# Kernel tuning notes

Hardware: AMD Instinct MI355X
Metric: run time of the kernel (lower is better)

The kernel has to match this reference:

```python
import jax, jax.numpy as jnp
import numpy as np

EMBED = 1024
HEADS = 16
HEAD_DIM = EMBED // HEADS


def setup_inputs() -> dict:
    key = jax.random.key(0)
    ks = jax.random.split(key, 8)
    N, S = 4, 2048
    inp = {
        "values": jax.random.normal(ks[0], (N, S, EMBED), jnp.float32),
        "keys": jax.random.normal(ks[1], (N, S, EMBED), jnp.float32),
        "queries": jax.random.normal(ks[2], (N, S, EMBED), jnp.float32),
        "mask": jnp.ones((N, S), jnp.int32),  # unused by the original forward
        # learned params (torch Linear: y = x @ W.T + b)
        "Wv": jax.random.normal(ks[3], (HEAD_DIM, HEAD_DIM), jnp.float32) / np.sqrt(HEAD_DIM),
        "Wk": jax.random.normal(ks[4], (HEAD_DIM, HEAD_DIM), jnp.float32) / np.sqrt(HEAD_DIM),
        "Wq": jax.random.normal(ks[5], (HEAD_DIM, HEAD_DIM), jnp.float32) / np.sqrt(HEAD_DIM),
        "Wo": jax.random.normal(ks[6], (EMBED, EMBED), jnp.float32) / np.sqrt(EMBED),
        "bo": jax.random.normal(ks[7], (EMBED,), jnp.float32) * 0.01,
    }
    return inp


def reference(values, keys, queries, mask, Wv, Wk, Wq, Wo, bo):
    N, S, _ = queries.shape
    # reshape to (N, len, heads, head_dim)
    v = values.reshape(N, S, HEADS, HEAD_DIM)
    k = keys.reshape(N, S, HEADS, HEAD_DIM)
    q = queries.reshape(N, S, HEADS, HEAD_DIM)
    # per-head linear projections (weights shared across heads), y = x @ W.T
    v = jnp.einsum('nlhd,ed->nlhe', v, Wv)
    k = jnp.einsum('nlhd,ed->nlhe', k, Wk)
    q = jnp.einsum('nlhd,ed->nlhe', q, Wq)
    # attention scores scaled by sqrt(embed_size), faithful to original
    scores = jnp.einsum('nqhd,nkhd->nhqk', q, k) / jnp.sqrt(jnp.float32(EMBED))
    attn = jax.nn.softmax(scores, axis=3)
    out = jnp.einsum('nhql,nlhd->nqhd', attn, v).reshape(N, S, EMBED)
    return out @ Wo.T + bo
```

## Files before the change

kernel.cpp:

```cpp
#include <hip/hip_runtime.h>


using f32x4  = __attribute__((ext_vector_type(4))) float;
using f32x16 = __attribute__((ext_vector_type(16))) float;
using bf16x8 = __attribute__((ext_vector_type(8))) __bf16;
using u32x4  = __attribute__((ext_vector_type(4))) unsigned int;
using u16x8  = __attribute__((ext_vector_type(8))) unsigned short;
typedef unsigned short u16;
typedef unsigned int   u32;
typedef unsigned long long u64;

#define SEQ 2048
#define EMB 1024
#define NHEADS 16
#define HDIM 64
#define NBATCH 4
#define NH 64

__device__ __forceinline__ u16 f2bf(float f) {
  u32 u = __builtin_bit_cast(u32, f);
  return (u16)((u + 0x7fffu + ((u >> 16) & 1u)) >> 16);
}

__device__ __forceinline__ u32 cvtpk_bf16(float a, float b) {
  u32 d;
  asm("v_cvt_pk_bf16_f32 %0, %1, %2" : "=v"(d) : "v"(a), "v"(b));
  return d;
}

__device__ __forceinline__ f32x4 mfma16(bf16x8 a, bf16x8 b, f32x4 c) {
  return __builtin_amdgcn_mfma_f32_16x16x32_bf16(a, b, c, 0, 0, 0);
}

__device__ __forceinline__ f32x16 mfma32(bf16x8 a, bf16x8 b, f32x16 c) {
  return __builtin_amdgcn_mfma_f32_32x32x16_bf16(a, b, c, 0, 0, 0);
}

__device__ __forceinline__ bf16x8 cvt8(f32x4 a, f32x4 b) {
  u32x4 r;
  r[0] = cvtpk_bf16(a[0], a[1]);
  r[1] = cvtpk_bf16(a[2], a[3]);
  r[2] = cvtpk_bf16(b[0], b[1]);
  r[3] = cvtpk_bf16(b[2], b[3]);
  return __builtin_bit_cast(bf16x8, r);
}

__device__ __forceinline__ float fexp2(float x) {
#if __has_builtin(__builtin_amdgcn_exp2f)
  return __builtin_amdgcn_exp2f(x);
#else
  return __expf(x * 0.6931471805599453f);
#endif
}

__device__ __forceinline__ void swap_words(u32 a, u32 b, int hi, u32& wlo, u32& whi) {
#if __has_builtin(__builtin_amdgcn_permlane32_swap)
  (void)hi;
  auto rr = __builtin_amdgcn_permlane32_swap((int)a, (int)b, false, false);
  wlo = (u32)rr[0];
  whi = (u32)rr[1];
#else
  u32 pa = (u32)__shfl_xor((int)a, 32);
  u32 pb = (u32)__shfl_xor((int)b, 32);
  wlo = hi ? pb : a;
  whi = hi ? b : pa;
#endif
}

__global__ __launch_bounds__(256) void proj_kernel(
    const float* __restrict__ Xq, const float* __restrict__ Xk, const float* __restrict__ Xv,
    const float* __restrict__ Wq, const float* __restrict__ Wk, const float* __restrict__ Wv,
    u16* __restrict__ Qp, u16* __restrict__ Kp, u16* __restrict__ Vp)
{
  int which = blockIdx.y;
  const float* X = which == 0 ? Xq : (which == 1 ? Xk : Xv);
  const float* W = which == 0 ? Wq : (which == 1 ? Wk : Wv);
  u16* Out = which == 0 ? Qp : (which == 1 ? Kp : Vp);
  float wscale = which == 0 ? 0.045084220027780106f : 1.0f;

  int t = threadIdx.x;
  int w = t >> 6, l = t & 63, l15 = l & 15, grp = l >> 4;
  int g0 = blockIdx.x * 64;

  bf16x8 wf[4][2];
#pragma unroll
  for (int nt = 0; nt < 4; nt++) {
    int c = nt * 16 + l15;
#pragma unroll
    for (int dc = 0; dc < 2; dc++) {
      const float* p = W + c * 64 + dc * 32 + grp * 8;
      f32x4 a = *(const f32x4*)p;
      f32x4 b = *(const f32x4*)(p + 4);
      a *= wscale; b *= wscale;
      wf[nt][dc] = cvt8(a, b);
    }
  }
  int grow = g0 + w * 16 + l15;
  const float* xr = X + (long)grow * 64;
  bf16x8 af[2];
#pragma unroll
  for (int dc = 0; dc < 2; dc++) {
    f32x4 a = *(const f32x4*)(xr + dc * 32 + grp * 8);
    f32x4 b = *(const f32x4*)(xr + dc * 32 + grp * 8 + 4);
    af[dc] = cvt8(a, b);
  }
  f32x4 acc[4] = {};
#pragma unroll
  for (int dc = 0; dc < 2; dc++)
#pragma unroll
    for (int nt = 0; nt < 4; nt++)
      acc[nt] = mfma16(af[dc], wf[nt][dc], acc[nt]);

#pragma unroll
  for (int r = 0; r < 4; r++) {
    int g = g0 + w * 16 + grp * 4 + r;
    int n = g >> 15;
    int s = (g >> 4) & 2047;
    int h = g & 15;
    u16* orow = Out + (((long)(n * NHEADS + h) * SEQ + s) << 6);
#pragma unroll
    for (int nt = 0; nt < 4; nt++)
      orow[nt * 16 + l15] = f2bf(acc[nt][r]);
  }
}

__global__ __launch_bounds__(256) void transpose_v(
    const u16* __restrict__ Vp, u16* __restrict__ Vt)
{
  int st = blockIdx.x;
  int nh = blockIdx.y;
  __shared__ u16 Vs[64 * 65];
  int t = threadIdx.x;
  const u16* src = Vp + ((long)nh * SEQ + st * 64) * 64;
#pragma unroll
  for (int p = 0; p < 2; p++) {
    int row = p * 32 + (t >> 3);
    int c0 = (t & 7) * 8;
    u32x4 u = *(const u32x4*)(src + row * 64 + c0);
    u16x8 v = __builtin_bit_cast(u16x8, u);
#pragma unroll
    for (int j = 0; j < 8; j++) Vs[(c0 + j) * 65 + row] = v[j];
  }
  __syncthreads();
  int e = t >> 2, k0 = (t & 3) * 16;
  u16x8 lo, hi;
#pragma unroll
  for (int j = 0; j < 8; j++) { lo[j] = Vs[e * 65 + k0 + j]; hi[j] = Vs[e * 65 + k0 + 8 + j]; }
  u16* dst = Vt + ((long)nh * 64 + e) * SEQ + st * 64 + k0;
  *(u32x4*)dst = __builtin_bit_cast(u32x4, lo);
  *(u32x4*)(dst + 8) = __builtin_bit_cast(u32x4, hi);
}

__global__ __launch_bounds__(256) void conv_wo(
    const float* __restrict__ Wo, u16* __restrict__ Wob)
{
  int i = (blockIdx.x * 256 + threadIdx.x) * 4;
  f32x4 v = *(const f32x4*)(Wo + i);
  u32 w0 = cvtpk_bf16(v[0], v[1]);
  u32 w1 = cvtpk_bf16(v[2], v[3]);
  u64 pk = (u64)w0 | ((u64)w1 << 32);
  *(u64*)(Wob + i) = pk;
}


#define LDV(off) __builtin_bit_cast(bf16x8, *(const u32x4*)(smem + (off)))

#define ATTN_STEP(CUROFF, DOSTAGE, DOPREF) do {                            \
    f32x16 zz = {};                                                        \
    f32x16 s0, s1;                                                         \
    __builtin_amdgcn_s_setprio(1);                                         \
    {                                                                      \
      bf16x8 kf0 = LDV(koff[0] + (CUROFF));                                \
      bf16x8 kf1 = LDV(koff[1] + (CUROFF));                                \
      s0 = mfma32(kf0, qf[0], zz);                                         \
      s1 = mfma32(kf1, qf[0], zz);                                         \
    }                                                                      \
    _Pragma("unroll")                                                      \
    for (int dc = 1; dc < 4; dc++) {                                       \
      bf16x8 kf0 = LDV(koff[dc * 2 + 0] + (CUROFF));                       \
      bf16x8 kf1 = LDV(koff[dc * 2 + 1] + (CUROFF));                       \
      s0 = mfma32(kf0, qf[dc], s0);                                        \
      s1 = mfma32(kf1, qf[dc], s1);                                        \
    }                                                                      \
    __builtin_amdgcn_s_setprio(0);                                         \
    if (DOSTAGE) {                                                         \
      *(u32x4*)(smem + sphys0 + ((CUROFF) ^ 16384)) = kreg[0];             \
      *(u32x4*)(smem + sphys1 + ((CUROFF) ^ 16384)) = kreg[1];             \
      *(u32x4*)(smem + sphys0 + 8192 + ((CUROFF) ^ 16384)) = vreg[0];      \
      *(u32x4*)(smem + sphys1 + 8192 + ((CUROFF) ^ 16384)) = vreg[1];      \
      if (DOPREF) {                                                        \
        kreg[0] = *(const u32x4*)kp0; kp0 += 8192;                         \
        kreg[1] = *(const u32x4*)kp1; kp1 += 8192;                         \
        vreg[0] = *(const u32x4*)vp0; vp0 += 128;                          \
        vreg[1] = *(const u32x4*)vp1; vp1 += 128;                          \
      }                                                                    \
    }                                                                      \
                                    \
    _Pragma("unroll")                                                      \
    for (int r = 0; r < 16; r++) s0[r] = fexp2(s0[r]);                     \
    _Pragma("unroll")                                                      \
    for (int r = 0; r < 16; r++) s1[r] = fexp2(s1[r]);                     \
    { f32x16 ss = s0 + s1;                                                 \
      f32x4 q4 = { ss[0]+ss[4], ss[1]+ss[5], ss[2]+ss[6], ss[3]+ss[7] };   \
      f32x4 q5 = { ss[8]+ss[12], ss[9]+ss[13], ss[10]+ss[14], ss[11]+ss[15] }; \
      f32x4 q6 = q4 + q5;                                                  \
      lrun += (q6[0] + q6[1]) + (q6[2] + q6[3]); }                         \
              \
    bf16x8 pB[4];                                                          \
    { u32 xw[8], wq[16];                                                   \
      _Pragma("unroll")                                                    \
      for (int i = 0; i < 8; i++) xw[i] = cvtpk_bf16(s0[2*i], s0[2*i+1]);  \
      swap_words(xw[0], xw[2], hi, wq[0], wq[2]);                          \
      swap_words(xw[1], xw[3], hi, wq[1], wq[3]);                          \
      swap_words(xw[4], xw[6], hi, wq[4], wq[6]);                          \
      swap_words(xw[5], xw[7], hi, wq[5], wq[7]);                          \
      _Pragma("unroll")                                                    \
      for (int i = 0; i < 8; i++) xw[i] = cvtpk_bf16(s1[2*i], s1[2*i+1]);  \
      swap_words(xw[0], xw[2], hi, wq[8], wq[10]);                         \
      swap_words(xw[1], xw[3], hi, wq[9], wq[11]);                         \
      swap_words(xw[4], xw[6], hi, wq[12], wq[14]);                        \
      swap_words(xw[5], xw[7], hi, wq[13], wq[15]);                        \
      _Pragma("unroll")                                                    \
      for (int kb = 0; kb < 4; kb++) {                                     \
        u32x4 v4 = { wq[kb*4+0], wq[kb*4+1], wq[kb*4+2], wq[kb*4+3] };     \
        pB[kb] = __builtin_bit_cast(bf16x8, v4); } }                       \
                                                 \
    __builtin_amdgcn_s_setprio(1);                                         \
    _Pragma("unroll")                                                      \
    for (int kb = 0; kb < 4; kb++) {                                       \
      bf16x8 vf0 = LDV(koff[kb * 2 + 0] + 8192 + (CUROFF));                \
      bf16x8 vf1 = LDV(koff[kb * 2 + 1] + 8192 + (CUROFF));                \
      o0 = mfma32(vf0, pB[kb], o0);                                        \
      o1 = mfma32(vf1, pB[kb], o1);                                        \
    }                                                                      \
    __builtin_amdgcn_s_setprio(0);                                         \
    __syncthreads();                                                       \
  } while (0)

__global__ __launch_bounds__(256, 3) void attn_kernel(
    const u16* __restrict__ Qp, const u16* __restrict__ Kp, const u16* __restrict__ Vt,
    u16* __restrict__ AO)
{
  int nh = blockIdx.x;
  int qb = blockIdx.y;
  int n = nh >> 4, h = nh & 15;

  __shared__ __align__(16) char smem[32768];

  int t = threadIdx.x, w = t >> 6, l = t & 63;
  int l31 = l & 31, hi = l >> 5;

  long qrow = (long)nh * SEQ + qb * 128 + w * 32 + l31;
  const char* qbase = (const char*)Qp + qrow * 128;
  bf16x8 qf[4];
#pragma unroll
  for (int dc = 0; dc < 4; dc++)
    qf[dc] = __builtin_bit_cast(bf16x8, *(const u32x4*)(qbase + dc * 32 + hi * 16));

  f32x16 o0 = {}, o1 = {};
  float lrun = 0.f;

  int koff[8];
#pragma unroll
  for (int dc = 0; dc < 4; dc++)
#pragma unroll
    for (int half = 0; half < 2; half++) {
      int row = half * 32 + l31;
      int cc = dc * 2 + hi;
      koff[dc * 2 + half] = row * 128 + ((cc ^ (row & 7)) << 4);
    }

  int sr0 = t >> 3, sc = t & 7, sr1 = sr0 + 32;
  int sphys0 = sr0 * 128 + ((sc ^ (sr0 & 7)) << 4);
  int sphys1 = sr1 * 128 + ((sc ^ (sr1 & 7)) << 4);

  const char* Kg = (const char*)(Kp + (long)nh * SEQ * 64);
  const char* Vg = (const char*)(Vt + (long)nh * 64 * SEQ);
  const char* kp0 = Kg + sr0 * 128 + sc * 16;
  const char* kp1 = Kg + sr1 * 128 + sc * 16;
  const char* vp0 = Vg + (long)sr0 * 4096 + sc * 16;
  const char* vp1 = Vg + (long)sr1 * 4096 + sc * 16;

  u32x4 kreg[2], vreg[2];
  kreg[0] = *(const u32x4*)kp0;
  kreg[1] = *(const u32x4*)kp1;
  vreg[0] = *(const u32x4*)vp0;
  vreg[1] = *(const u32x4*)vp1;
  *(u32x4*)(smem + sphys0) = kreg[0];
  *(u32x4*)(smem + sphys1) = kreg[1];
  *(u32x4*)(smem + 8192 + sphys0) = vreg[0];
  *(u32x4*)(smem + 8192 + sphys1) = vreg[1];
  kreg[0] = *(const u32x4*)(kp0 + 8192); kp0 += 16384;
  kreg[1] = *(const u32x4*)(kp1 + 8192); kp1 += 16384;
  vreg[0] = *(const u32x4*)(vp0 + 128);  vp0 += 256;
  vreg[1] = *(const u32x4*)(vp1 + 128);  vp1 += 256;
  __syncthreads();

  for (int kt2 = 0; kt2 < 16; kt2++) {
    ATTN_STEP(0, true, (kt2 < 15));
    ATTN_STEP(16384, (kt2 < 15), (kt2 < 15));
  }

  lrun += __shfl_xor(lrun, 32);
  float inv = 1.0f / lrun;
  int qlocal = w * 32 + l31;
  char* OsmB = smem;
#pragma unroll
  for (int i = 0; i < 8; i++) {
    int e0 = ((2 * i) & 3) + 8 * ((2 * i) >> 2) + 4 * hi;
    *(u32*)(OsmB + qlocal * 144 + 2 * e0) = cvtpk_bf16(o0[2*i] * inv, o0[2*i+1] * inv);
    *(u32*)(OsmB + qlocal * 144 + 2 * (e0 + 32)) = cvtpk_bf16(o1[2*i] * inv, o1[2*i+1] * inv);
  }
  __syncthreads();
  int qr = t >> 1, half = t & 1;
  const char* src = OsmB + qr * 144 + half * 64;
  long qg = (long)qb * 128 + qr;
  char* dst = (char*)(AO + ((long)n * SEQ + qg) * EMB + h * 64 + half * 32);
#pragma unroll
  for (int j = 0; j < 4; j++)
    *(u32x4*)(dst + j * 16) = *(const u32x4*)(src + j * 16);
}

__global__ __launch_bounds__(256) void gemm_out(
    const u16* __restrict__ A, const u16* __restrict__ B,
    const float* __restrict__ bias, float* __restrict__ C)
{
  int bm0 = blockIdx.x;
  int bm = (bm0 & 7) * 8 + (bm0 >> 3);
  int bn = blockIdx.y;
  __shared__ __align__(16) char gsm[32768];
  int t = threadIdx.x, w = t >> 6, l = t & 63;
  int l31 = l & 31, hi = l >> 5;
  int wm = w >> 1, wn = w & 1;
  f32x16 acc[2][2] = {};
  const char* Ab = (const char*)(A + (long)bm * 128 * 1024);
  const char* Bb = (const char*)(B + (long)bn * 128 * 1024);

  int srow = t >> 2, sc2 = t & 3;
  int srow1 = srow + 64;
  int sp0 = srow * 64 + ((sc2 ^ ((srow >> 1) & 3)) << 4);
  int sp1 = srow1 * 64 + ((sc2 ^ ((srow1 >> 1) & 3)) << 4);

  int aoff[2][2], boff[2][2];
#pragma unroll
  for (int ti = 0; ti < 2; ti++)
#pragma unroll
    for (int kk = 0; kk < 2; kk++) {
      int rowa = wm * 64 + ti * 32 + l31;
      int rowb = wn * 64 + ti * 32 + l31;
      int c = kk * 2 + hi;
      aoff[ti][kk] = rowa * 64 + ((c ^ ((rowa >> 1) & 3)) << 4);
      boff[ti][kk] = 8192 + rowb * 64 + ((c ^ ((rowb >> 1) & 3)) << 4);
    }

  u32x4 areg[2], breg[2];
  areg[0] = *(const u32x4*)(Ab + (long)srow * 2048 + sc2 * 16);
  areg[1] = *(const u32x4*)(Ab + (long)srow1 * 2048 + sc2 * 16);
  breg[0] = *(const u32x4*)(Bb + (long)srow * 2048 + sc2 * 16);
  breg[1] = *(const u32x4*)(Bb + (long)srow1 * 2048 + sc2 * 16);
  *(u32x4*)(gsm + sp0) = areg[0];
  *(u32x4*)(gsm + sp1) = areg[1];
  *(u32x4*)(gsm + 8192 + sp0) = breg[0];
  *(u32x4*)(gsm + 8192 + sp1) = breg[1];
  areg[0] = *(const u32x4*)(Ab + (long)srow * 2048 + 64 + sc2 * 16);
  areg[1] = *(const u32x4*)(Ab + (long)srow1 * 2048 + 64 + sc2 * 16);
  breg[0] = *(const u32x4*)(Bb + (long)srow * 2048 + 64 + sc2 * 16);
  breg[1] = *(const u32x4*)(Bb + (long)srow1 * 2048 + 64 + sc2 * 16);
  __syncthreads();

  for (int kt = 0; kt < 32; kt++) {
    const char* cur = gsm + ((kt & 1) << 14);
    char* nxt = gsm + (((kt + 1) & 1) << 14);

    bf16x8 af[2][2], bf_[2][2];
#pragma unroll
    for (int ti = 0; ti < 2; ti++)
#pragma unroll
      for (int kk = 0; kk < 2; kk++) {
        af[ti][kk] = __builtin_bit_cast(bf16x8, *(const u32x4*)(cur + aoff[ti][kk]));
        bf_[ti][kk] = __builtin_bit_cast(bf16x8, *(const u32x4*)(cur + boff[ti][kk]));
      }

    if (kt + 1 < 32) {
      *(u32x4*)(nxt + sp0) = areg[0];
      *(u32x4*)(nxt + sp1) = areg[1];
      *(u32x4*)(nxt + 8192 + sp0) = breg[0];
      *(u32x4*)(nxt + 8192 + sp1) = breg[1];
      if (kt + 2 < 32) {
        areg[0] = *(const u32x4*)(Ab + (long)srow * 2048 + (kt + 2) * 64 + sc2 * 16);
        areg[1] = *(const u32x4*)(Ab + (long)srow1 * 2048 + (kt + 2) * 64 + sc2 * 16);
        breg[0] = *(const u32x4*)(Bb + (long)srow * 2048 + (kt + 2) * 64 + sc2 * 16);
        breg[1] = *(const u32x4*)(Bb + (long)srow1 * 2048 + (kt + 2) * 64 + sc2 * 16);
      }
    }

    __builtin_amdgcn_s_setprio(1);
#pragma unroll
    for (int ti = 0; ti < 2; ti++)
#pragma unroll
      for (int tj = 0; tj < 2; tj++) {
        acc[ti][tj] = mfma32(af[ti][0], bf_[tj][0], acc[ti][tj]);
        acc[ti][tj] = mfma32(af[ti][1], bf_[tj][1], acc[ti][tj]);
      }
    __builtin_amdgcn_s_setprio(0);

    __syncthreads();
  }

  float bv[2];
#pragma unroll
  for (int tj = 0; tj < 2; tj++) bv[tj] = bias[bn * 128 + wn * 64 + tj * 32 + l31];
#pragma unroll
  for (int ti = 0; ti < 2; ti++)
#pragma unroll
    for (int tj = 0; tj < 2; tj++) {
#pragma unroll
      for (int r = 0; r < 16; r++) {
        long row = (long)bm * 128 + wm * 64 + ti * 32 + ((r & 3) + 8 * (r >> 2) + 4 * hi);
        C[row * 1024 + bn * 128 + wn * 64 + tj * 32 + l31] = acc[ti][tj][r] + bv[tj];
      }
    }
}

extern "C" void kernel_launch(void* const* d_in, const int* in_sizes, int n_in,
                              void* d_out, int out_size, void* d_ws, size_t ws_size,
                              hipStream_t stream)
{
  const float* Vx = (const float*)d_in[0];
  const float* Kx = (const float*)d_in[1];
  const float* Qx = (const float*)d_in[2];
  const float* Wv = (const float*)d_in[4];
  const float* Wk = (const float*)d_in[5];
  const float* Wq = (const float*)d_in[6];
  const float* Wo = (const float*)d_in[7];
  const float* bo = (const float*)d_in[8];
  float* out = (float*)d_out;
  char* ws = (char*)d_ws;

  u16* Qp  = (u16*)(ws);
  u16* Kp  = (u16*)(ws + (1L << 24));
  u16* Vt  = (u16*)(ws + (2L << 24));
  u16* Vp  = (u16*)(ws + (3L << 24));
  u16* AO  = Vp;
  u16* Wob = (u16*)(ws + (4L << 24));

  proj_kernel<<<dim3(2048, 3), 256, 0, stream>>>(Qx, Kx, Vx, Wq, Wk, Wv, Qp, Kp, Vp);
  transpose_v<<<dim3(32, 64), 256, 0, stream>>>(Vp, Vt);
  conv_wo<<<1024, 256, 0, stream>>>(Wo, Wob);
  attn_kernel<<<dim3(64, 16), 256, 0, stream>>>(Qp, Kp, Vt, AO);
  gemm_out<<<dim3(64, 8), 256, 0, stream>>>(AO, Wob, bo, out);
}
```

Before: 176.9 us.

## Stage projection outputs through LDS and double gemm_out K-tile depth

The projection kernel now writes its bf16 results into a padded shared-memory tile, then emits full 64-byte row segments with 16-byte vector stores, replacing scattered 2-byte global stores. The output GEMM doubles its K tile from 32 to 64 per iteration, which halves the number of loop iterations and barriers. It also switches to a 128-byte-row XOR swizzle and interleaves LDS fragment reads with the MFMAs. In exchange, gemm_out's shared memory grows to 64KB and it holds more prefetch registers, which may reduce occupancy.

```diff
diff --git a/kernel.cpp b/kernel.cpp
--- a/kernel.cpp
+++ b/kernel.cpp
@@ -78,6 +78,8 @@
   u16* Out = which == 0 ? Qp : (which == 1 ? Kp : Vp);
   float wscale = which == 0 ? 0.045084220027780106f : 1.0f;
 
+  __shared__ u16 Osm[64 * 72];
+
   int t = threadIdx.x;
   int w = t >> 6, l = t & 63, l15 = l & 15, grp = l >> 4;
   int g0 = blockIdx.x * 64;
@@ -112,16 +114,20 @@
       acc[nt] = mfma16(af[dc], wf[nt][dc], acc[nt]);
 
 #pragma unroll
-  for (int r = 0; r < 4; r++) {
-    int g = g0 + w * 16 + grp * 4 + r;
-    int n = g >> 15;
-    int s = (g >> 4) & 2047;
-    int h = g & 15;
-    u16* orow = Out + (((long)(n * NHEADS + h) * SEQ + s) << 6);
+  for (int r = 0; r < 4; r++)
 #pragma unroll
     for (int nt = 0; nt < 4; nt++)
-      orow[nt * 16 + l15] = f2bf(acc[nt][r]);
-  }
+      Osm[(w * 16 + grp * 4 + r) * 72 + nt * 16 + l15] = f2bf(acc[nt][r]);
+
+  int rl = t >> 2, qtr = t & 3;
+  const char* srcp = (const char*)Osm + rl * 144 + qtr * 32;
+  u32x4 v0 = *(const u32x4*)srcp;
+  u32x4 v1 = *(const u32x4*)(srcp + 16);
+  int g = g0 + rl;
+  int n = g >> 15, s = (g >> 4) & 2047, h = g & 15;
+  char* dstp = (char*)(Out + (((long)(n * NHEADS + h) * SEQ + s) << 6)) + qtr * 32;
+  *(u32x4*)dstp = v0;
+  *(u32x4*)(dstp + 16) = v1;
 }
 
 __global__ __launch_bounds__(256) void transpose_v(
@@ -328,7 +334,7 @@
   int bm0 = blockIdx.x;
   int bm = (bm0 & 7) * 8 + (bm0 >> 3);
   int bn = blockIdx.y;
-  __shared__ __align__(16) char gsm[32768];
+  __shared__ __align__(16) char gsm[65536];
   int t = threadIdx.x, w = t >> 6, l = t & 63;
   int l31 = l & 31, hi = l >> 5;
   int wm = w >> 1, wn = w & 1;
@@ -336,72 +342,77 @@
   const char* Ab = (const char*)(A + (long)bm * 128 * 1024);
   const char* Bb = (const char*)(B + (long)bn * 128 * 1024);
 
-  int srow = t >> 2, sc2 = t & 3;
-  int srow1 = srow + 64;
-  int sp0 = srow * 64 + ((sc2 ^ ((srow >> 1) & 3)) << 4);
-  int sp1 = srow1 * 64 + ((sc2 ^ ((srow1 >> 1) & 3)) << 4);
-
-  int aoff[2][2], boff[2][2];
+  int cphys[4];
+  long cgoff[4];
+#pragma unroll
+  for (int p = 0; p < 4; p++) {
+    int i = t + p * 256;
+    int row = i >> 3, c = i & 7;
+    cphys[p] = row * 128 + ((c ^ (row & 7)) << 4);
+    cgoff[p] = (long)row * 2048 + c * 16;
+  }
+
+  int aoff[2][4], boff[2][4];
 #pragma unroll
   for (int ti = 0; ti < 2; ti++)
 #pragma unroll
-    for (int kk = 0; kk < 2; kk++) {
+    for (int kk = 0; kk < 4; kk++) {
       int rowa = wm * 64 + ti * 32 + l31;
       int rowb = wn * 64 + ti * 32 + l31;
       int c = kk * 2 + hi;
-      aoff[ti][kk] = rowa * 64 + ((c ^ ((rowa >> 1) & 3)) << 4);
-      boff[ti][kk] = 8192 + rowb * 64 + ((c ^ ((rowb >> 1) & 3)) << 4);
-    }
-
-  u32x4 areg[2], breg[2];
-  areg[0] = *(const u32x4*)(Ab + (long)srow * 2048 + sc2 * 16);
-  areg[1] = *(const u32x4*)(Ab + (long)srow1 * 2048 + sc2 * 16);
-  breg[0] = *(const u32x4*)(Bb + (long)srow * 2048 + sc2 * 16);
-  breg[1] = *(const u32x4*)(Bb + (long)srow1 * 2048 + sc2 * 16);
-  *(u32x4*)(gsm + sp0) = areg[0];
-  *(u32x4*)(gsm + sp1) = areg[1];
-  *(u32x4*)(gsm + 8192 + sp0) = breg[0];
-  *(u32x4*)(gsm + 8192 + sp1) = breg[1];
-  areg[0] = *(const u32x4*)(Ab + (long)srow * 2048 + 64 + sc2 * 16);
-  areg[1] = *(const u32x4*)(Ab + (long)srow1 * 2048 + 64 + sc2 * 16);
-  breg[0] = *(const u32x4*)(Bb + (long)srow * 2048 + 64 + sc2 * 16);
-  breg[1] = *(const u32x4*)(Bb + (long)srow1 * 2048 + 64 + sc2 * 16);
+      aoff[ti][kk] = rowa * 128 + ((c ^ (rowa & 7)) << 4);
+      boff[ti][kk] = 16384 + rowb * 128 + ((c ^ (rowb & 7)) << 4);
+    }
+
+  u32x4 areg[4], breg[4];
+#pragma unroll
+  for (int p = 0; p < 4; p++) {
+    areg[p] = *(const u32x4*)(Ab + cgoff[p]);
+    breg[p] = *(const u32x4*)(Bb + cgoff[p]);
+  }
+#pragma unroll
+  for (int p = 0; p < 4; p++) {
+    *(u32x4*)(gsm + cphys[p]) = areg[p];
+    *(u32x4*)(gsm + 16384 + cphys[p]) = breg[p];
+  }
+#pragma unroll
+  for (int p = 0; p < 4; p++) {
+    areg[p] = *(const u32x4*)(Ab + cgoff[p] + 128);
+    breg[p] = *(const u32x4*)(Bb + cgoff[p] + 128);
+  }
   __syncthreads();
 
-  for (int kt = 0; kt < 32; kt++) {
-    const char* cur = gsm + ((kt & 1) << 14);
-    char* nxt = gsm + (((kt + 1) & 1) << 14);
-
-    bf16x8 af[2][2], bf_[2][2];
-#pragma unroll
-    for (int ti = 0; ti < 2; ti++)
-#pragma unroll
-      for (int kk = 0; kk < 2; kk++) {
-        af[ti][kk] = __builtin_bit_cast(bf16x8, *(const u32x4*)(cur + aoff[ti][kk]));
-        bf_[ti][kk] = __builtin_bit_cast(bf16x8, *(const u32x4*)(cur + boff[ti][kk]));
+  for (int kt = 0; kt < 16; kt++) {
+    const char* cur = gsm + ((kt & 1) << 15);
+    char* nxt = gsm + (((kt + 1) & 1) << 15);
+
+    if (kt + 1 < 16) {
+#pragma unroll
+      for (int p = 0; p < 4; p++) {
+        *(u32x4*)(nxt + cphys[p]) = areg[p];
+        *(u32x4*)(nxt + 16384 + cphys[p]) = breg[p];
       }
-
-    if (kt + 1 < 32) {
-      *(u32x4*)(nxt + sp0) = areg[0];
-      *(u32x4*)(nxt + sp1) = areg[1];
-      *(u32x4*)(nxt + 8192 + sp0) = breg[0];
-      *(u32x4*)(nxt + 8192 + sp1) = breg[1];
-      if (kt + 2 < 32) {
-        areg[0] = *(const u32x4*)(Ab + (long)srow * 2048 + (kt + 2) * 64 + sc2 * 16);
-        areg[1] = *(const u32x4*)(Ab + (long)srow1 * 2048 + (kt + 2) * 64 + sc2 * 16);
-        breg[0] = *(const u32x4*)(Bb + (long)srow * 2048 + (kt + 2) * 64 + sc2 * 16);
-        breg[1] = *(const u32x4*)(Bb + (long)srow1 * 2048 + (kt + 2) * 64 + sc2 * 16);
+      if (kt + 2 < 16) {
+#pragma unroll
+        for (int p = 0; p < 4; p++) {
+          areg[p] = *(const u32x4*)(Ab + cgoff[p] + (kt + 2) * 128);
+          breg[p] = *(const u32x4*)(Bb + cgoff[p] + (kt + 2) * 128);
+        }
       }
     }
 
     __builtin_amdgcn_s_setprio(1);
 #pragma unroll
-    for (int ti = 0; ti < 2; ti++)
-#pragma unroll
-      for (int tj = 0; tj < 2; tj++) {
-        acc[ti][tj] = mfma32(af[ti][0], bf_[tj][0], acc[ti][tj]);
-        acc[ti][tj] = mfma32(af[ti][1], bf_[tj][1], acc[ti][tj]);
-      }
+    for (int kk = 0; kk < 4; kk++) {
+      bf16x8 af0 = __builtin_bit_cast(bf16x8, *(const u32x4*)(cur + aoff[0][kk]));
+      bf16x8 af1 = __builtin_bit_cast(bf16x8, *(const u32x4*)(cur + aoff[1][kk]));
+      bf16x8 bf0 = __builtin_bit_cast(bf16x8, *(const u32x4*)(cur + boff[0][kk]));
+      bf16x8 bf1 = __builtin_bit_cast(bf16x8, *(const u32x4*)(cur + boff[1][kk]));
+      acc[0][0] = mfma32(af0, bf0, acc[0][0]);
+      acc[0][1] = mfma32(af0, bf1, acc[0][1]);
+      acc[1][0] = mfma32(af1, bf0, acc[1][0]);
+      acc[1][1] = mfma32(af1, bf1, acc[1][1]);
+    }
     __builtin_amdgcn_s_setprio(0);
 
     __syncthreads();
```

Measured after the change: 174.6 us. About the same (-1.3%).
